# Optimization experiments

Hardware: AMD Instinct MI355X
Metric: run time of the kernel (lower is better)

## Reference

```python
import math
import jax, jax.numpy as jnp
import numpy as np

V, H, NH, L, P = 50257, 768, 12, 6, 2048
DH = H // NH
EPS = 1e-12


def _ln(x, g, b):
    m = jnp.mean(x, axis=-1, keepdims=True)
    v = jnp.var(x, axis=-1, keepdims=True)
    return (x - m) * jax.lax.rsqrt(v + EPS) * g + b


def setup_inputs() -> dict:
    key = jax.random.key(0)
    ks = jax.random.split(key, 16)
    s = 0.02
    inp = {
        "input_ids": jax.random.randint(ks[0], (2, 2048), 0, V),
        "wte": jax.random.normal(ks[1], (V, H), jnp.float32) * s,
        "wpe": jax.random.normal(ks[2], (P, H), jnp.float32) * s,
        "ln1_g": jnp.ones((L, H), jnp.float32),
        "ln1_b": jnp.zeros((L, H), jnp.float32),
        "qkv_w": jax.random.normal(ks[3], (L, H, 3 * H), jnp.float32) * s,
        "qkv_b": jnp.zeros((L, 3 * H), jnp.float32),
        "dense_w": jax.random.normal(ks[4], (L, H, H), jnp.float32) * (s / math.sqrt(2 * L)),
        "dense_b": jnp.zeros((L, H), jnp.float32),
        "ln2_g": jnp.ones((L, H), jnp.float32),
        "ln2_b": jnp.zeros((L, H), jnp.float32),
        "fc1_w": jax.random.normal(ks[5], (L, H, 2 * H), jnp.float32) * s,
        "fc2_w": jax.random.normal(ks[6], (L, 2 * H, H), jnp.float32) * (s / math.sqrt(2 * L)),
        "fc2_b": jnp.zeros((L, H), jnp.float32),
        "lnf_g": jnp.ones((H,), jnp.float32),
        "lnf_b": jnp.zeros((H,), jnp.float32),
    }
    return inp


def _gpt(input_ids, wte, wpe, ln1_g, ln1_b, qkv_w, qkv_b, dense_w, dense_b,
         ln2_g, ln2_b, fc1_w, fc2_w, fc2_b, lnf_g, lnf_b):
    B, S = input_ids.shape
    x = wte[input_ids] + wpe[:S][None]  # [B,S,H]
    causal = jnp.tril(jnp.ones((S, S), bool))  # [S,S]

    def block(x, p):
        g1, b1, qw, qb, dw, db, g2, b2, f1w, f2w, f2b = p
        h = _ln(x, g1, b1)
        qkv = h @ qw + qb  # [B,S,3H]
        q, k, v = jnp.split(qkv, 3, axis=-1)
        q = q.reshape(B, S, NH, DH).transpose(0, 2, 1, 3)
        k = k.reshape(B, S, NH, DH).transpose(0, 2, 1, 3)
        v = v.reshape(B, S, NH, DH).transpose(0, 2, 1, 3)
        scores = jnp.einsum('bhqd,bhkd->bhqk', q, k) / math.sqrt(DH)
        scores = jnp.where(causal, scores, -jnp.inf)
        probs = jax.nn.softmax(scores, axis=-1)
        out = jnp.einsum('bhqk,bhkd->bhqd', probs, v)
        out = out.transpose(0, 2, 1, 3).reshape(B, S, H)
        x = x + out @ dw + db
        h2 = _ln(x, g2, b2)
        mlp = jax.nn.gelu(h2 @ f1w, approximate=False) @ f2w + f2b
        return x + mlp, None

    params = (ln1_g, ln1_b, qkv_w, qkv_b, dense_w, dense_b,
              ln2_g, ln2_b, fc1_w, fc2_w, fc2_b)
    x, _ = jax.lax.scan(block, x, params)
    x = _ln(x, lnf_g, lnf_b)
    # targets=None path: logits for last position only, tied lm head
    return x[:, -1:, :] @ wte.T  # [B,1,V]


def reference(input_ids, wte, wpe, ln1_g, ln1_b, qkv_w, qkv_b, dense_w, dense_b,
              ln2_g, ln2_b, fc1_w, fc2_w, fc2_b, lnf_g, lnf_b):
    return _gpt(input_ids, wte, wpe, ln1_g, ln1_b, qkv_w, qkv_b, dense_w, dense_b,
                ln2_g, ln2_b, fc1_w, fc2_w, fc2_b, lnf_g, lnf_b)
```

## Files before the change

### kernel.cpp

```cpp
#include <hip/hip_runtime.h>
#include <math.h>

#define H 768
#define NH 12
#define DH 64
#define SEQ 2048
#define BATCH 2
#define TOK (BATCH*SEQ)
#define LAYERS 6
#define VOCAB 50257

#define WOFF_QKV   0
#define WSZ_QKV    (2304*768)
#define WOFF_DENSE (WOFF_QKV + WSZ_QKV)
#define WSZ_DENSE  (768*768)
#define WOFF_FC1   (WOFF_DENSE + WSZ_DENSE)
#define WSZ_FC1    (1536*768)
#define WOFF_FC2   (WOFF_FC1 + WSZ_FC1)
#define WSZ_FC2    (768*1536)
#define WSTRIDE    (WOFF_FC2 + WSZ_FC2)

typedef __attribute__((ext_vector_type(8))) short short8;
typedef __attribute__((ext_vector_type(4))) float floatx4;

__device__ __forceinline__ float bf2f(unsigned short u) {
    union { unsigned int i; float f; } v; v.i = ((unsigned int)u) << 16; return v.f;
}
__device__ __forceinline__ unsigned short f2b(float f) {
    union { float f; unsigned int i; } v; v.f = f;
    unsigned int u = v.i;
    return (unsigned short)((u + 0x7FFFu + ((u >> 16) & 1u)) >> 16);
}
__device__ __forceinline__ void gload_lds16(const void* g, void* lds) {
    __builtin_amdgcn_global_load_lds((const __attribute__((address_space(1))) unsigned int*)g,
                                     (__attribute__((address_space(3))) unsigned int*)lds,
                                     16, 0, 0);
}

__global__ __launch_bounds__(256) void embed_kernel(const int* __restrict__ ids,
                                                    const float* __restrict__ wte,
                                                    const float* __restrict__ wpe,
                                                    float* __restrict__ x) {
    int row = blockIdx.x;
    int s = row & (SEQ - 1);
    int id = ids[row];
    const float* wrow = wte + (size_t)id * H;
    const float* prow = wpe + (size_t)s * H;
    float* xrow = x + (size_t)row * H;
    for (int i = threadIdx.x; i < H; i += 256)
        xrow[i] = wrow[i] + prow[i];
}

template <bool BF>
__global__ __launch_bounds__(256) void ln_kernel(const float* __restrict__ x,
                                                 const float* __restrict__ g,
                                                 const float* __restrict__ bb,
                                                 void* __restrict__ outv,
                                                 int rs, int ro) {
    __shared__ float red[4];
    __shared__ float mean_s, rstd_s;
    int row = blockIdx.x * rs + ro;
    const float* xr = x + (size_t)row * H;
    int t = threadIdx.x;
    float v0 = xr[t], v1 = xr[t + 256], v2 = xr[t + 512];
    float s = v0 + v1 + v2;
    #pragma unroll
    for (int off = 32; off > 0; off >>= 1) s += __shfl_down(s, off);
    int lane = t & 63, wid = t >> 6;
    if (lane == 0) red[wid] = s;
    __syncthreads();
    if (t == 0) mean_s = (red[0] + red[1] + red[2] + red[3]) * (1.0f / 768.0f);
    __syncthreads();
    float m = mean_s;
    float d0 = v0 - m, d1 = v1 - m, d2 = v2 - m;
    float q = d0 * d0 + d1 * d1 + d2 * d2;
    #pragma unroll
    for (int off = 32; off > 0; off >>= 1) q += __shfl_down(q, off);
    if (lane == 0) red[wid] = q;
    __syncthreads();
    if (t == 0) rstd_s = rsqrtf((red[0] + red[1] + red[2] + red[3]) * (1.0f / 768.0f) + 1e-12f);
    __syncthreads();
    float r = rstd_s;
    float o0 = d0 * r * g[t]       + bb[t];
    float o1 = d1 * r * g[t + 256] + bb[t + 256];
    float o2 = d2 * r * g[t + 512] + bb[t + 512];
    if (BF) {
        unsigned short* orow = (unsigned short*)outv + (size_t)blockIdx.x * H;
        orow[t] = f2b(o0); orow[t + 256] = f2b(o1); orow[t + 512] = f2b(o2);
    } else {
        float* orow = (float*)outv + (size_t)blockIdx.x * H;
        orow[t] = o0; orow[t + 256] = o1; orow[t + 512] = o2;
    }
}

__global__ __launch_bounds__(256) void wconv_all(const float* __restrict__ qkv_w,
                                                 const float* __restrict__ dense_w,
                                                 const float* __restrict__ fc1_w,
                                                 const float* __restrict__ fc2_w,
                                                 unsigned short* __restrict__ wt) {
    __shared__ float tile[64][65];
    int bid = blockIdx.x;
    int l = bid / 1152;
    int r = bid % 1152;
    const float* W; unsigned short* D; int K, N, tn, tk;
    if (r < 432)      { W = qkv_w  + (size_t)l * 768 * 2304; D = wt + (size_t)l * WSTRIDE + WOFF_QKV;
                        K = 768;  N = 2304; tn = r % 36; tk = r / 36; }
    else if (r < 576) { r -= 432; W = dense_w + (size_t)l * 768 * 768; D = wt + (size_t)l * WSTRIDE + WOFF_DENSE;
                        K = 768;  N = 768;  tn = r % 12; tk = r / 12; }
    else if (r < 864) { r -= 576; W = fc1_w + (size_t)l * 768 * 1536; D = wt + (size_t)l * WSTRIDE + WOFF_FC1;
                        K = 768;  N = 1536; tn = r % 24; tk = r / 24; }
    else              { r -= 864; W = fc2_w + (size_t)l * 1536 * 768; D = wt + (size_t)l * WSTRIDE + WOFF_FC2;
                        K = 1536; N = 768;  tn = r % 12; tk = r / 12; }
    int n0 = tn * 64, k0 = tk * 64;
    int t = threadIdx.x;
    int rr = t >> 4, c = (t & 15) << 2;
    #pragma unroll
    for (int i = 0; i < 4; ++i) {
        float4 v = *(const float4*)(W + (size_t)(k0 + rr + 16 * i) * N + n0 + c);
        tile[rr + 16 * i][c + 0] = v.x; tile[rr + 16 * i][c + 1] = v.y;
        tile[rr + 16 * i][c + 2] = v.z; tile[rr + 16 * i][c + 3] = v.w;
    }
    __syncthreads();
    #pragma unroll
    for (int i = 0; i < 4; ++i) {
        int n = rr + 16 * i;
        ushort4 o;
        o.x = f2b(tile[c + 0][n]); o.y = f2b(tile[c + 1][n]);
        o.z = f2b(tile[c + 2][n]); o.w = f2b(tile[c + 3][n]);
        *(ushort4*)(D + (size_t)(n0 + n) * K + k0 + c) = o;
    }
}

#define GBK 32
template <int TM, int TN, int MODE>
__global__ __launch_bounds__(256) void gemm_bf16(const unsigned short* __restrict__ A,
                                                 const unsigned short* __restrict__ Bt,
                                                 const float* __restrict__ bias,
                                                 const float* __restrict__ res,
                                                 void* __restrict__ Cv,
                                                 unsigned short* __restrict__ vtb,
                                                 int M, int N, int K) {
    constexpr int MI = TM / 32, NI = TN / 32;
    __shared__ short As[2][TM * GBK];
    __shared__ short Bs[2][TN * GBK];
    int t = threadIdx.x;
    int w = t >> 6, lane = t & 63;
    int wr = w >> 1, wc = w & 1;
    int l16 = lane & 15, quad = lane >> 4;
    int bm = blockIdx.y * TM, bn = blockIdx.x * TN;

    floatx4 acc[MI][NI] = {};
    int srow = lane >> 2;
    int scol = (lane & 3) * 8;
    const unsigned short* Aw[TM / 64];
    const unsigned short* Bw[TN / 64];
    #pragma unroll
    for (int j = 0; j < TM / 64; ++j)
        Aw[j] = A + (size_t)(bm + w * (TM / 4) + j * 16 + srow) * K + scol;
    #pragma unroll
    for (int j = 0; j < TN / 64; ++j)
        Bw[j] = Bt + (size_t)(bn + w * (TN / 4) + j * 16 + srow) * K + scol;

    auto stage = [&](int b, int k0) {
        #pragma unroll
        for (int j = 0; j < TM / 64; ++j)
            gload_lds16(Aw[j] + k0, (char*)&As[b][0] + (w * (TM / 4) + j * 16) * 64);
        #pragma unroll
        for (int j = 0; j < TN / 64; ++j)
            gload_lds16(Bw[j] + k0, (char*)&Bs[b][0] + (w * (TN / 4) + j * 16) * 64);
    };
    auto compute = [&](int b) {
        short8 af[MI], bfr[NI];
        #pragma unroll
        for (int mi = 0; mi < MI; ++mi)
            af[mi] = *(const short8*)&As[b][(wr * (TM / 2) + mi * 16 + l16) * GBK + quad * 8];
        #pragma unroll
        for (int ni = 0; ni < NI; ++ni)
            bfr[ni] = *(const short8*)&Bs[b][(wc * (TN / 2) + ni * 16 + l16) * GBK + quad * 8];
        #pragma unroll
        for (int mi = 0; mi < MI; ++mi)
            #pragma unroll
            for (int ni = 0; ni < NI; ++ni)
                acc[mi][ni] = __builtin_amdgcn_mfma_f32_16x16x32_bf16(af[mi], bfr[ni], acc[mi][ni], 0, 0, 0);
    };

    stage(0, 0);
    __syncthreads();
    const int KT = K / GBK;
    for (int kt = 0; kt < KT; kt += 2) {
        stage(1, (kt + 1) * GBK);
        compute(0);
        __syncthreads();
        if (kt + 2 < KT) stage(0, (kt + 2) * GBK);
        compute(1);
        __syncthreads();
    }

    int r0 = bm + wr * (TM / 2) + quad * 4;
    int c0 = bn + wc * (TN / 2) + l16;
    #pragma unroll
    for (int ni = 0; ni < NI; ++ni) {
        int gc = c0 + ni * 16;
        float bv = (MODE != 2) ? bias[gc] : 0.0f;
        #pragma unroll
        for (int mi = 0; mi < MI; ++mi) {
            int gr = r0 + mi * 16;
            if (MODE == 0 && gc >= 1536) {
                int hd = gc - 1536;
                int bb_ = gr >> 11, ss = gr & 2047;
                ushort4 o4;
                o4.x = f2b(acc[mi][ni][0] + bv);
                o4.y = f2b(acc[mi][ni][1] + bv);
                o4.z = f2b(acc[mi][ni][2] + bv);
                o4.w = f2b(acc[mi][ni][3] + bv);
                *(ushort4*)&vtb[((size_t)(bb_ * NH + (hd >> 6)) * 64 + (hd & 63)) * SEQ + ss] = o4;
            } else {
                #pragma unroll
                for (int reg = 0; reg < 4; ++reg) {
                    float v = acc[mi][ni][reg];
                    size_t idx = (size_t)(gr + reg) * N + gc;
                    if (MODE == 2) {
                        v = 0.5f * v * (1.0f + erff(v * 0.70710678118654752f));
                        ((unsigned short*)Cv)[idx] = f2b(v);
                    } else if (MODE == 0) {
                        v += bv;
                        if (gc < 768) v *= 0.125f;
                        ((unsigned short*)Cv)[idx] = f2b(v);
                    } else {
                        ((float*)Cv)[idx] = v + bv + res[idx];
                    }
                }
            }
        }
    }
}

#define ATQ 64
#define ATK 64
#define PTP 72
#define NQTA (SEQ/ATQ)
__global__ __launch_bounds__(256) void attn_mfma(const unsigned short* __restrict__ qkv,
                                                 const unsigned short* __restrict__ vt,
                                                 unsigned short* __restrict__ out) {
    __shared__ unsigned short Qs[ATQ * 64];
    __shared__ unsigned short Ks[2][ATK * 64];
    __shared__ unsigned short Vts[2][64 * ATK];
    __shared__ unsigned short Pt[4][16 * PTP];

    int idx = blockIdx.x;
    int bh = idx % (BATCH * NH);
    int qt_blk = (NQTA - 1) - idx / (BATCH * NH);
    int b = bh / NH, hh = bh % NH;
    int qbase = qt_blk * ATQ;
    const size_t rstride = 3 * H;
    const unsigned short* base = qkv + (size_t)b * SEQ * rstride;
    const unsigned short* vbase = vt + (size_t)bh * DH * SEQ;

    int t = threadIdx.x;
    int w = t >> 6, lane = t & 63;
    int l16 = lane & 15, quad = lane >> 4;
    int lrow = lane >> 3;
    int swsrc = ((lane & 7) ^ lrow) * 8;
    int l7 = l16 & 7;

    auto stageKV = [&](int bb, int kt) {
        int k0 = kt * ATK;
        #pragma unroll
        for (int i = 0; i < 2; ++i) {
            int row = w * 16 + i * 8 + lrow;
            gload_lds16(base + (size_t)(k0 + row) * rstride + H + hh * 64 + swsrc,
                        (unsigned short*)Ks[bb] + w * 1024 + i * 512);
            gload_lds16(vbase + (size_t)row * SEQ + k0 + swsrc,
                        (unsigned short*)Vts[bb] + w * 1024 + i * 512);
        }
    };

    #pragma unroll
    for (int i = 0; i < 2; ++i) {
        int row = w * 16 + i * 8 + lrow;
        gload_lds16(base + (size_t)(qbase + row) * rstride + hh * 64 + swsrc,
                    Qs + w * 1024 + i * 512);
    }
    stageKV(0, 0);
    __syncthreads();

    short8 qf[2];
    #pragma unroll
    for (int ch = 0; ch < 2; ++ch)
        qf[ch] = *(const short8*)&Qs[(w * 16 + l16) * 64 + ((ch * 4 + quad) ^ l7) * 8];

    float mst = -INFINITY;
    float lst = 0.0f;
    floatx4 oacc[4] = {};

    auto computeTile = [&](int bb, int kt) {
        int k0 = kt * ATK;
        floatx4 sacc[4] = {};
        __builtin_amdgcn_s_setprio(1);
        #pragma unroll
        for (int ch = 0; ch < 2; ++ch) {
            short8 kf[4];
            #pragma unroll
            for (int i = 0; i < 4; ++i)
                kf[i] = *(const short8*)&Ks[bb][(i * 16 + l16) * 64 + ((ch * 4 + quad) ^ l7) * 8];
            #pragma unroll
            for (int i = 0; i < 4; ++i)
                sacc[i] = __builtin_amdgcn_mfma_f32_16x16x32_bf16(kf[i], qf[ch], sacc[i], 0, 0, 0);
        }
        __builtin_amdgcn_s_setprio(0);

        bool needmask = (k0 + ATK - 1) > (qbase + w * 16);
        int qg = qbase + w * 16 + l16;
        float tm = -INFINITY;
        #pragma unroll
        for (int i = 0; i < 4; ++i)
            #pragma unroll
            for (int r = 0; r < 4; ++r) {
                float v = sacc[i][r];
                int kg = k0 + i * 16 + quad * 4 + r;
                if (needmask && kg > qg) v = -INFINITY;
                sacc[i][r] = v;
                tm = fmaxf(tm, v);
            }
        tm = fmaxf(tm, __shfl_xor(tm, 16));
        tm = fmaxf(tm, __shfl_xor(tm, 32));
        float mold = mst;
        float mnew = fmaxf(mold, tm);
        float alpha = __expf(mold - mnew);
        float suml = 0.0f;
        #pragma unroll
        for (int i = 0; i < 4; ++i) {
            float e0 = __expf(sacc[i][0] - mnew);
            float e1 = __expf(sacc[i][1] - mnew);
            float e2 = __expf(sacc[i][2] - mnew);
            float e3 = __expf(sacc[i][3] - mnew);
            suml += (e0 + e1) + (e2 + e3);
            uint2 u;
            u.x = (unsigned int)f2b(e0) | ((unsigned int)f2b(e1) << 16);
            u.y = (unsigned int)f2b(e2) | ((unsigned int)f2b(e3) << 16);
            *(uint2*)&Pt[w][l16 * PTP + i * 16 + quad * 4] = u;
        }
        suml += __shfl_xor(suml, 16);
        suml += __shfl_xor(suml, 32);
        lst = lst * alpha + suml;
        mst = mnew;
        #pragma unroll
        for (int r = 0; r < 4; ++r) {
            float ab = __shfl(alpha, quad * 4 + r);
            #pragma unroll
            for (int dt = 0; dt < 4; ++dt) oacc[dt][r] *= ab;
        }

        __builtin_amdgcn_s_setprio(1);
        #pragma unroll
        for (int ch = 0; ch < 2; ++ch) {
            short8 pf = *(const short8*)&Pt[w][l16 * PTP + ch * 32 + quad * 8];
            short8 vf[4];
            #pragma unroll
            for (int dt = 0; dt < 4; ++dt)
                vf[dt] = *(const short8*)&Vts[bb][(dt * 16 + l16) * 64 + ((ch * 4 + quad) ^ l7) * 8];
            #pragma unroll
            for (int dt = 0; dt < 4; ++dt)
                oacc[dt] = __builtin_amdgcn_mfma_f32_16x16x32_bf16(pf, vf[dt], oacc[dt], 0, 0, 0);
        }
        __builtin_amdgcn_s_setprio(0);
    };

    int ntiles = qt_blk + 1;
    for (int kt = 0; kt < ntiles; kt += 2) {
        if (kt + 1 < ntiles) stageKV(1, kt + 1);
        computeTile(0, kt);
        __syncthreads();
        if (kt + 1 < ntiles) {
            if (kt + 2 < ntiles) stageKV(0, kt + 2);
            computeTile(1, kt + 1);
            __syncthreads();
        }
    }

    #pragma unroll
    for (int r = 0; r < 4; ++r) {
        float lr = __shfl(lst, quad * 4 + r);
        float inv = 1.0f / lr;
        int qg = qbase + w * 16 + quad * 4 + r;
        #pragma unroll
        for (int dt = 0; dt < 4; ++dt)
            out[(size_t)(b * SEQ + qg) * H + hh * 64 + dt * 16 + l16] =
                f2b(oacc[dt][r] * inv);
    }
}

__global__ __launch_bounds__(256) void logits_kernel(const float* __restrict__ xf,
                                                     const float* __restrict__ wte,
                                                     float* __restrict__ out) {
    int v = blockIdx.x * 4 + (threadIdx.x >> 6);
    if (v >= VOCAB) return;
    int lane = threadIdx.x & 63;
    const float* w = wte + (size_t)v * H + lane * 4;
    const float* x0 = xf + lane * 4;
    const float* x1 = xf + H + lane * 4;
    float4 w0 = *(const float4*)(w);
    float4 w1 = *(const float4*)(w + 256);
    float4 w2 = *(const float4*)(w + 512);
    float4 a0 = *(const float4*)(x0);
    float4 a1 = *(const float4*)(x0 + 256);
    float4 a2 = *(const float4*)(x0 + 512);
    float4 b0 = *(const float4*)(x1);
    float4 b1 = *(const float4*)(x1 + 256);
    float4 b2 = *(const float4*)(x1 + 512);
    float s0 = w0.x*a0.x + w0.y*a0.y + w0.z*a0.z + w0.w*a0.w
             + w1.x*a1.x + w1.y*a1.y + w1.z*a1.z + w1.w*a1.w
             + w2.x*a2.x + w2.y*a2.y + w2.z*a2.z + w2.w*a2.w;
    float s1 = w0.x*b0.x + w0.y*b0.y + w0.z*b0.z + w0.w*b0.w
             + w1.x*b1.x + w1.y*b1.y + w1.z*b1.z + w1.w*b1.w
             + w2.x*b2.x + w2.y*b2.y + w2.z*b2.z + w2.w*b2.w;
    #pragma unroll
    for (int off = 32; off > 0; off >>= 1) {
        s0 += __shfl_down(s0, off);
        s1 += __shfl_down(s1, off);
    }
    if (lane == 0) {
        out[v] = s0;
        out[VOCAB + v] = s1;
    }
}

extern "C" void kernel_launch(void* const* d_in, const int* in_sizes, int n_in,
                              void* d_out, int out_size, void* d_ws, size_t ws_size,
                              hipStream_t stream) {
    const int*   ids     = (const int*)d_in[0];
    const float* wte     = (const float*)d_in[1];
    const float* wpe     = (const float*)d_in[2];
    const float* ln1_g   = (const float*)d_in[3];
    const float* ln1_b   = (const float*)d_in[4];
    const float* qkv_w   = (const float*)d_in[5];
    const float* qkv_b   = (const float*)d_in[6];
    const float* dense_w = (const float*)d_in[7];
    const float* dense_b = (const float*)d_in[8];
    const float* ln2_g   = (const float*)d_in[9];
    const float* ln2_b   = (const float*)d_in[10];
    const float* fc1_w   = (const float*)d_in[11];
    const float* fc2_w   = (const float*)d_in[12];
    const float* fc2_b   = (const float*)d_in[13];
    const float* lnf_g   = (const float*)d_in[14];
    const float* lnf_b   = (const float*)d_in[15];
    float* outp = (float*)d_out;

    char* p = (char*)d_ws;
    float* x             = (float*)p;          p += (size_t)TOK * H * 4;
    unsigned short* h    = (unsigned short*)p; p += (size_t)TOK * H * 2;
    unsigned short* qkvb = (unsigned short*)p; p += (size_t)TOK * 3 * H * 2;
    unsigned short* attnb= (unsigned short*)p; p += (size_t)TOK * H * 2;
    unsigned short* ab   = (unsigned short*)p; p += (size_t)TOK * 2 * H * 2;
    unsigned short* wt   = (unsigned short*)p; p += (size_t)WSTRIDE * LAYERS * 2;
    float* xf            = (float*)p;          p += (size_t)BATCH * H * 4;
    unsigned short* vtb  = ab;

    embed_kernel<<<TOK, 256, 0, stream>>>(ids, wte, wpe, x);
    wconv_all<<<LAYERS * 1152, 256, 0, stream>>>(qkv_w, dense_w, fc1_w, fc2_w, wt);

    for (int l = 0; l < LAYERS; ++l) {
        const unsigned short* wl = wt + (size_t)l * WSTRIDE;
        ln_kernel<true><<<TOK, 256, 0, stream>>>(x, ln1_g + l * H, ln1_b + l * H, h, 1, 0);
        gemm_bf16<128, 128, 0><<<dim3(2304 / 128, TOK / 128), 256, 0, stream>>>(
            h, wl + WOFF_QKV, qkv_b + l * 3 * H, nullptr, qkvb, vtb, TOK, 2304, 768);
        attn_mfma<<<BATCH * NH * NQTA, 256, 0, stream>>>(qkvb, vtb, attnb);
        gemm_bf16<64, 64, 1><<<dim3(768 / 64, TOK / 64), 256, 0, stream>>>(
            attnb, wl + WOFF_DENSE, dense_b + l * H, x, x, nullptr, TOK, 768, 768);
        ln_kernel<true><<<TOK, 256, 0, stream>>>(x, ln2_g + l * H, ln2_b + l * H, h, 1, 0);
        gemm_bf16<64, 128, 2><<<dim3(1536 / 128, TOK / 64), 256, 0, stream>>>(
            h, wl + WOFF_FC1, nullptr, nullptr, ab, nullptr, TOK, 1536, 768);
        gemm_bf16<64, 64, 1><<<dim3(768 / 64, TOK / 64), 256, 0, stream>>>(
            ab, wl + WOFF_FC2, fc2_b + l * H, x, x, nullptr, TOK, 768, 1536);
    }

    ln_kernel<false><<<BATCH, 256, 0, stream>>>(x, lnf_g, lnf_b, xf, SEQ, SEQ - 1);
    logits_kernel<<<(VOCAB + 3) / 4, 256, 0, stream>>>(xf, wte, outp);
}
```

Baseline: 1.354 ms.

## Double GEMM K-tile to 64 with XOR-swizzled LDS layout and smaller QKV tile

The bf16 GEMM now stages a K depth of 64 per iteration instead of 32, so each tile issues two MFMA k-steps per barrier. Global-to-LDS loads use 8 rows per wave-load, and the 16-byte column chunks are XOR-swizzled by row to avoid LDS bank conflicts on fragment reads. The QKV projection switches from 128x128 to 64x128 tiles, which doubles its grid for better CU occupancy. The change halves the number of barriers per K, at the cost of more LDS per block and a more complex addressing scheme.

After: 1.215 ms. 1.11x faster.

```diff
diff --git a/kernel.cpp b/kernel.cpp
--- a/kernel.cpp
+++ b/kernel.cpp
@@ -131,7 +131,7 @@
     }
 }
 
-#define GBK 32
+#define GBK 64
 template <int TM, int TN, int MODE>
 __global__ __launch_bounds__(256) void gemm_bf16(const unsigned short* __restrict__ A,
                                                  const unsigned short* __restrict__ Bt,
@@ -141,47 +141,54 @@
                                                  unsigned short* __restrict__ vtb,
                                                  int M, int N, int K) {
     constexpr int MI = TM / 32, NI = TN / 32;
+    constexpr int ALD = TM / 32, BLD = TN / 32;
     __shared__ short As[2][TM * GBK];
     __shared__ short Bs[2][TN * GBK];
     int t = threadIdx.x;
     int w = t >> 6, lane = t & 63;
     int wr = w >> 1, wc = w & 1;
     int l16 = lane & 15, quad = lane >> 4;
+    int l7 = l16 & 7;
+    int lrow = lane >> 3;
+    int swsrc = ((lane & 7) ^ lrow) * 8;
     int bm = blockIdx.y * TM, bn = blockIdx.x * TN;
 
     floatx4 acc[MI][NI] = {};
-    int srow = lane >> 2;
-    int scol = (lane & 3) * 8;
-    const unsigned short* Aw[TM / 64];
-    const unsigned short* Bw[TN / 64];
-    #pragma unroll
-    for (int j = 0; j < TM / 64; ++j)
-        Aw[j] = A + (size_t)(bm + w * (TM / 4) + j * 16 + srow) * K + scol;
-    #pragma unroll
-    for (int j = 0; j < TN / 64; ++j)
-        Bw[j] = Bt + (size_t)(bn + w * (TN / 4) + j * 16 + srow) * K + scol;
+    const unsigned short* Aw[ALD];
+    const unsigned short* Bw[BLD];
+    #pragma unroll
+    for (int j = 0; j < ALD; ++j)
+        Aw[j] = A + (size_t)(bm + w * (TM / 4) + j * 8 + lrow) * K + swsrc;
+    #pragma unroll
+    for (int j = 0; j < BLD; ++j)
+        Bw[j] = Bt + (size_t)(bn + w * (TN / 4) + j * 8 + lrow) * K + swsrc;
 
     auto stage = [&](int b, int k0) {
         #pragma unroll
-        for (int j = 0; j < TM / 64; ++j)
-            gload_lds16(Aw[j] + k0, (char*)&As[b][0] + (w * (TM / 4) + j * 16) * 64);
-        #pragma unroll
-        for (int j = 0; j < TN / 64; ++j)
-            gload_lds16(Bw[j] + k0, (char*)&Bs[b][0] + (w * (TN / 4) + j * 16) * 64);
+        for (int j = 0; j < ALD; ++j)
+            gload_lds16(Aw[j] + k0, (char*)&As[b][0] + (w * (TM / 4) + j * 8) * (GBK * 2));
+        #pragma unroll
+        for (int j = 0; j < BLD; ++j)
+            gload_lds16(Bw[j] + k0, (char*)&Bs[b][0] + (w * (TN / 4) + j * 8) * (GBK * 2));
     };
     auto compute = [&](int b) {
-        short8 af[MI], bfr[NI];
-        #pragma unroll
-        for (int mi = 0; mi < MI; ++mi)
-            af[mi] = *(const short8*)&As[b][(wr * (TM / 2) + mi * 16 + l16) * GBK + quad * 8];
-        #pragma unroll
-        for (int ni = 0; ni < NI; ++ni)
-            bfr[ni] = *(const short8*)&Bs[b][(wc * (TN / 2) + ni * 16 + l16) * GBK + quad * 8];
-        #pragma unroll
-        for (int mi = 0; mi < MI; ++mi)
+        short8 af[2][MI], bfr[2][NI];
+        #pragma unroll
+        for (int kk = 0; kk < 2; ++kk) {
+            #pragma unroll
+            for (int mi = 0; mi < MI; ++mi)
+                af[kk][mi] = *(const short8*)&As[b][(wr * (TM / 2) + mi * 16 + l16) * GBK + ((kk * 4 + quad) ^ l7) * 8];
             #pragma unroll
             for (int ni = 0; ni < NI; ++ni)
-                acc[mi][ni] = __builtin_amdgcn_mfma_f32_16x16x32_bf16(af[mi], bfr[ni], acc[mi][ni], 0, 0, 0);
+                bfr[kk][ni] = *(const short8*)&Bs[b][(wc * (TN / 2) + ni * 16 + l16) * GBK + ((kk * 4 + quad) ^ l7) * 8];
+        }
+        #pragma unroll
+        for (int kk = 0; kk < 2; ++kk)
+            #pragma unroll
+            for (int mi = 0; mi < MI; ++mi)
+                #pragma unroll
+                for (int ni = 0; ni < NI; ++ni)
+                    acc[mi][ni] = __builtin_amdgcn_mfma_f32_16x16x32_bf16(af[kk][mi], bfr[kk][ni], acc[mi][ni], 0, 0, 0);
     };
 
     stage(0, 0);
@@ -462,7 +469,7 @@
     for (int l = 0; l < LAYERS; ++l) {
         const unsigned short* wl = wt + (size_t)l * WSTRIDE;
         ln_kernel<true><<<TOK, 256, 0, stream>>>(x, ln1_g + l * H, ln1_b + l * H, h, 1, 0);
-        gemm_bf16<128, 128, 0><<<dim3(2304 / 128, TOK / 128), 256, 0, stream>>>(
+        gemm_bf16<64, 128, 0><<<dim3(2304 / 128, TOK / 64), 256, 0, stream>>>(
             h, wl + WOFF_QKV, qkv_b + l * 3 * H, nullptr, qkvb, vtb, TOK, 2304, 768);
         attn_mfma<<<BATCH * NH * NQTA, 256, 0, stream>>>(qkvb, vtb, attnb);
         gemm_bf16<64, 64, 1><<<dim3(768 / 64, TOK / 64), 256, 0, stream>>>(
```
